# Kernel optimization log

Hardware: AMD Instinct MI355X
Metric: run time of the kernel (lower is better)

Reference implementation:

```python
import jax, jax.numpy as jnp
import numpy as np

N_SPK, M_UTT, D_EMB = 1024, 32, 512


def setup_inputs() -> dict:
    key = jax.random.key(0)
    k0, = jax.random.split(key, 1)
    embeddings = jax.random.normal(k0, (N_SPK, M_UTT, D_EMB), dtype=jnp.float32)
    return {
        "embeddings": embeddings,
        "w": jnp.asarray(5.0, dtype=jnp.float32),
        "b": jnp.asarray(1.0, dtype=jnp.float32),
        "N": N_SPK,
        "M": M_UTT,
    }


def reference(embeddings, w, b, N, M):
    # embeddings: [N, M, D]
    centroids = embeddings.mean(axis=1)          # [N, D]
    sum_ = embeddings.sum(axis=1)                # [N, D]
    e_flat = embeddings.reshape(N * M, -1)       # [NM, D]
    cosine_sim = e_flat @ centroids.T            # [NM, N]

    # Exclusive-centroid diagonal overwrite (faithful to source, including
    # the operator precedence: c_j = sum_[j] - e[j,k] / (1 - M)):
    #   diag[j,k] = (sum_[j] - e[j,k]/(1-M)) . e[j,k]
    inv = 1.0 / (1.0 - M)
    diag = (jnp.einsum('nmd,nd->nm', embeddings, sum_)
            - inv * jnp.sum(embeddings * embeddings, axis=-1))  # [N, M]

    rows = jnp.arange(N * M)
    cols = jnp.repeat(jnp.arange(N), M)          # label layout: [0]*M, [1]*M, ...
    cosine_sim = cosine_sim.at[rows, cols].set(diag.reshape(-1))

    logits = w * cosine_sim + b                  # [NM, N]
    # cross_entropy with labels = cols, mean reduction
    logz = jax.nn.logsumexp(logits, axis=-1)     # [NM]
    loss = jnp.mean(logz - logits[rows, cols])
    return loss
```

## Files before the change

kernel.cpp:

```cpp
#include <hip/hip_runtime.h>

#define N_SPK 1024
#define M_UTT 32
#define D_EMB 512
#define NROWS (N_SPK * M_UTT)

#define NEG_INF (-__builtin_inff())
#define MARGIN 25.0f

using f32x4 = __attribute__((ext_vector_type(4))) float;


__global__ __launch_bounds__(256)
void prep_kernel(const float* __restrict__ e,
                 float* __restrict__ sumf, float* __restrict__ ssqA,
                 float* __restrict__ dgl, float* __restrict__ c2A,
                 const float* __restrict__ wp, const float* __restrict__ bp,
                 float* __restrict__ out, int* __restrict__ count,
                 int* __restrict__ doneCnt) {
    __shared__ float csum[4][D_EMB];
    __shared__ float c2red[4];
    const int n = blockIdx.x;
    const int wv = threadIdx.x >> 6, l = threadIdx.x & 63;

    if (n == 0 && threadIdx.x == 0) { out[0] = 0.f; *count = 0; *doneCnt = 0; }

    float xs[8][8];
    float ssq[8];
    float cacc[8];
#pragma unroll
    for (int j = 0; j < 8; ++j) cacc[j] = 0.f;

#pragma unroll
    for (int mi = 0; mi < 8; ++mi) {
        const int m = mi * 4 + wv;
        const size_t row = (size_t)n * M_UTT + m;
        const float* p = e + row * D_EMB + l * 8;
        float4 x0 = *(const float4*)p;
        float4 x1 = *(const float4*)(p + 4);
        xs[mi][0] = x0.x; xs[mi][1] = x0.y; xs[mi][2] = x0.z; xs[mi][3] = x0.w;
        xs[mi][4] = x1.x; xs[mi][5] = x1.y; xs[mi][6] = x1.z; xs[mi][7] = x1.w;
        float sq = 0.f;
#pragma unroll
        for (int j = 0; j < 8; ++j) {
            float x = xs[mi][j];
            cacc[j] += x;
            sq = __builtin_fmaf(x, x, sq);
        }
#pragma unroll
        for (int off = 32; off; off >>= 1) sq += __shfl_xor(sq, off);
        ssq[mi] = sq;
        if (l == 0) ssqA[row] = sq;
    }

#pragma unroll
    for (int j = 0; j < 8; ++j) csum[wv][l * 8 + j] = cacc[j];
    __syncthreads();
    float c2acc = 0.f;
    for (int d = threadIdx.x; d < D_EMB; d += 256) {
        float s = csum[0][d] + csum[1][d] + csum[2][d] + csum[3][d];
        csum[0][d] = s;
        sumf[(size_t)n * D_EMB + d] = s;
        float c = s * (1.0f / M_UTT);
        c2acc = __builtin_fmaf(c, c, c2acc);
    }
#pragma unroll
    for (int off = 32; off; off >>= 1) c2acc += __shfl_xor(c2acc, off);
    if (l == 0) c2red[wv] = c2acc;
    __syncthreads();
    if (threadIdx.x == 0)
        c2A[n] = (c2red[0] + c2red[1]) + (c2red[2] + c2red[3]);

    float sv[8];
#pragma unroll
    for (int j = 0; j < 8; ++j) sv[j] = csum[0][l * 8 + j];
    const float w = wp[0], bb = bp[0];
#pragma unroll
    for (int mi = 0; mi < 8; ++mi) {
        float dg = 0.f;
#pragma unroll
        for (int j = 0; j < 8; ++j) dg = __builtin_fmaf(xs[mi][j], sv[j], dg);
#pragma unroll
        for (int off = 32; off; off >>= 1) dg += __shfl_xor(dg, off);
        if (l == 0) {
            const size_t row = (size_t)n * M_UTT + mi * 4 + wv;
            dgl[row] = __builtin_fmaf(w, dg + ssq[mi] * (1.0f / 31.0f), bb);
        }
    }
}

__global__ __launch_bounds__(256)
void select_kernel(const float* __restrict__ ssqA, const float* __restrict__ dgl,
                   const float* __restrict__ c2A,
                   const float* __restrict__ wp, const float* __restrict__ bp,
                   int* __restrict__ count, int* __restrict__ active) {
    __shared__ float red[4];
    float m = 0.f;
#pragma unroll
    for (int i = 0; i < 4; ++i)
        m = fmaxf(m, c2A[threadIdx.x + i * 256]);
#pragma unroll
    for (int off = 32; off; off >>= 1) m = fmaxf(m, __shfl_xor(m, off));
    if ((threadIdx.x & 63) == 0) red[threadIdx.x >> 6] = m;
    __syncthreads();
    const float c2 = fmaxf(fmaxf(red[0], red[1]), fmaxf(red[2], red[3]));
    const float Cmax = __builtin_sqrtf(c2);

    const int row = blockIdx.x * 256 + threadIdx.x;
    const float bound = __builtin_fmaf(
        __builtin_fabsf(wp[0]) * __builtin_sqrtf(ssqA[row]), Cmax, bp[0]);
    if (dgl[row] - bound < MARGIN) {
        int slot = atomicAdd(count, 1);
        active[slot] = row;
    }
}

__global__ __launch_bounds__(256)
void active_kernel(const float* __restrict__ e, const float* __restrict__ sumf,
                   const float* __restrict__ dgl,
                   const int* __restrict__ count, const int* __restrict__ active,
                   const float* __restrict__ wp, const float* __restrict__ bp,
                   float2* __restrict__ pmA, int* __restrict__ doneCnt,
                   float* __restrict__ out) {
    __shared__ float er[D_EMB];
    __shared__ float2 red2[4];
    __shared__ int lastFlag;
    const int tid = threadIdx.x;
    const int cnt = *count;
    if (cnt == 0) return;
    const float w = wp[0], bb = bp[0];

    const int xcd = blockIdx.x & 7;
    const int chunk = xcd >> 1;
    const int g = (blockIdx.x >> 3) * 2 + (xcd & 1);
    const int gstride = (gridDim.x >> 3) * 2;

    if (tid == 0) lastFlag = 0;
    int myItems = 0;

    for (int slot = g; slot < cnt; slot += gstride) {
        const int row = active[slot];
        __syncthreads();
        er[tid] = e[(size_t)row * D_EMB + tid];
        er[tid + 256] = e[(size_t)row * D_EMB + 256 + tid];
        __syncthreads();

        const int j = chunk * 256 + tid;
        const float* sp = sumf + (size_t)j * D_EMB;
        float d0 = 0.f, d1 = 0.f, d2 = 0.f, d3 = 0.f;
        for (int k = 0; k < D_EMB; k += 4) {
            float4 s4 = *(const float4*)(sp + k);
            d0 = __builtin_fmaf(er[k + 0], s4.x, d0);
            d1 = __builtin_fmaf(er[k + 1], s4.y, d1);
            d2 = __builtin_fmaf(er[k + 2], s4.z, d2);
            d3 = __builtin_fmaf(er[k + 3], s4.w, d3);
        }
        const float dot = (d0 + d1) + (d2 + d3);
        float lg = __builtin_fmaf(w, dot * (1.0f / M_UTT), bb);
        if (j == (row >> 5)) lg = dgl[row];

        float mx = lg;
#pragma unroll
        for (int off = 32; off; off >>= 1) mx = fmaxf(mx, __shfl_xor(mx, off));
        float ss = __expf(lg - mx);
#pragma unroll
        for (int off = 32; off; off >>= 1) ss += __shfl_xor(ss, off);
        if ((tid & 63) == 0) { float2 v; v.x = mx; v.y = ss; red2[tid >> 6] = v; }
        __syncthreads();
        if (tid == 0) {
            float M = fmaxf(fmaxf(red2[0].x, red2[1].x),
                            fmaxf(red2[2].x, red2[3].x));
            float S = red2[0].y * __expf(red2[0].x - M)
                    + red2[1].y * __expf(red2[1].x - M)
                    + red2[2].y * __expf(red2[2].x - M)
                    + red2[3].y * __expf(red2[3].x - M);
            float2 v; v.x = M; v.y = S;
            __hip_atomic_store((unsigned long long*)&pmA[slot * 4 + chunk],
                               __builtin_bit_cast(unsigned long long, v),
                               __ATOMIC_RELAXED, __HIP_MEMORY_SCOPE_AGENT);
        }
        ++myItems;
    }

    __syncthreads();
    if (tid == 0 && myItems > 0) {
        int old = __hip_atomic_fetch_add(doneCnt, myItems,
                                         __ATOMIC_ACQ_REL,
                                         __HIP_MEMORY_SCOPE_AGENT);
        if (old + myItems == cnt * 4) lastFlag = 1;
    }
    __syncthreads();

    if (lastFlag) {
        for (int slot = tid; slot < cnt; slot += 256) {
            float2 pm[4];
#pragma unroll
            for (int c = 0; c < 4; ++c) {
                unsigned long long bits = __hip_atomic_load(
                    (unsigned long long*)&pmA[slot * 4 + c],
                    __ATOMIC_RELAXED, __HIP_MEMORY_SCOPE_AGENT);
                pm[c] = __builtin_bit_cast(float2, bits);
            }
            float M = fmaxf(fmaxf(pm[0].x, pm[1].x), fmaxf(pm[2].x, pm[3].x));
            float S = pm[0].y * __expf(pm[0].x - M) + pm[1].y * __expf(pm[1].x - M)
                    + pm[2].y * __expf(pm[2].x - M) + pm[3].y * __expf(pm[3].x - M);
            float loss = M + __logf(S) - dgl[active[slot]];
            atomicAdd(out, loss * (1.0f / NROWS));
        }
    }
}


__global__ void centroid_kernel(const float* __restrict__ e,
                                float* __restrict__ cent) {
    int gid = blockIdx.x * 256 + threadIdx.x;
    int n = gid >> 9;
    int d = gid & 511;
    const float* p = e + ((size_t)n * M_UTT) * D_EMB + d;
    float s = 0.f;
#pragma unroll
    for (int m = 0; m < M_UTT; ++m) s += p[(size_t)m * D_EMB];
    cent[gid] = s * (1.0f / M_UTT);
}

__global__ void normsq_kernel(const float* __restrict__ e,
                              float* __restrict__ nsq) {
    int wv = threadIdx.x >> 6;
    int lane = threadIdx.x & 63;
    int row = blockIdx.x * 4 + wv;
    const float* p = e + (size_t)row * D_EMB + lane;
    float s = 0.f;
#pragma unroll
    for (int j = 0; j < 8; ++j) { float x = p[j * 64]; s += x * x; }
#pragma unroll
    for (int off = 32; off; off >>= 1) s += __shfl_xor(s, off);
    if (lane == 0) nsq[row] = s;
}

#define BR 64
#define BC 128
#define BK 16
#define TR 4
#define TC 8

__global__ __launch_bounds__(256, 2)
void ge2e_main(const float* __restrict__ e, const float* __restrict__ cent,
               const float* __restrict__ nsq, const float* __restrict__ wp,
               const float* __restrict__ bp, float* __restrict__ partials) {
    __shared__ float As[BK][BR];
    __shared__ float Bs[BK][BC];
    __shared__ float diagLs[BR];
    __shared__ float red[16];

    const int tid = threadIdx.x;
    const int tx = tid & 15;
    const int ty = tid >> 4;
    const int blk = blockIdx.x;
    const int r0 = blk * BR;

    const float w = *wp;
    const float bb = *bp;

    float m_run[TR], s_run[TR];
#pragma unroll
    for (int i = 0; i < TR; ++i) { m_run[i] = NEG_INF; s_run[i] = 0.f; }

    const int a_row = tid >> 2;
    const int a_k   = (tid & 3) * 4;
    const int b_col = tid >> 1;
    const int b_k   = (tid & 1) * 8;

    for (int ct = 0; ct < N_SPK / BC; ++ct) {
        const int c0 = ct * BC;
        float acc[TR][TC];
#pragma unroll
        for (int i = 0; i < TR; ++i)
#pragma unroll
            for (int j = 0; j < TC; ++j) acc[i][j] = 0.f;

        for (int kk = 0; kk < D_EMB; kk += BK) {
            __syncthreads();
            {
                float4 av = *(const float4*)(e + (size_t)(r0 + a_row) * D_EMB + kk + a_k);
                As[a_k + 0][a_row] = av.x;
                As[a_k + 1][a_row] = av.y;
                As[a_k + 2][a_row] = av.z;
                As[a_k + 3][a_row] = av.w;
            }
            {
                const float* bp0 = cent + (size_t)(c0 + b_col) * D_EMB + kk + b_k;
                float4 bv0 = *(const float4*)(bp0);
                float4 bv1 = *(const float4*)(bp0 + 4);
                Bs[b_k + 0][b_col] = bv0.x;
                Bs[b_k + 1][b_col] = bv0.y;
                Bs[b_k + 2][b_col] = bv0.z;
                Bs[b_k + 3][b_col] = bv0.w;
                Bs[b_k + 4][b_col] = bv1.x;
                Bs[b_k + 5][b_col] = bv1.y;
                Bs[b_k + 6][b_col] = bv1.z;
                Bs[b_k + 7][b_col] = bv1.w;
            }
            __syncthreads();

#pragma unroll
            for (int k = 0; k < BK; ++k) {
                float4 a4 = *(const float4*)&As[k][ty * TR];
                float4 b4a = *(const float4*)&Bs[k][tx * TC];
                float4 b4b = *(const float4*)&Bs[k][tx * TC + 4];
                float av[TR] = {a4.x, a4.y, a4.z, a4.w};
                float bv[TC] = {b4a.x, b4a.y, b4a.z, b4a.w,
                                b4b.x, b4b.y, b4b.z, b4b.w};
#pragma unroll
                for (int i = 0; i < TR; ++i)
#pragma unroll
                    for (int j = 0; j < TC; ++j)
                        acc[i][j] = __builtin_fmaf(av[i], bv[j], acc[i][j]);
            }
        }

#pragma unroll
        for (int i = 0; i < TR; ++i) {
            const int grow = r0 + ty * TR + i;
            const int dcol = grow >> 5;
            float lv[TC];
#pragma unroll
            for (int j = 0; j < TC; ++j) {
                const int gcol = c0 + tx * TC + j;
                float v = acc[i][j];
                float lg;
                if (gcol == dcol) {
                    lg = __builtin_fmaf(w, __builtin_fmaf(32.0f, v,
                             (1.0f / 31.0f) * nsq[grow]), bb);
                    diagLs[ty * TR + i] = lg;
                } else {
                    lg = __builtin_fmaf(w, v, bb);
                }
                lv[j] = lg;
            }
            float mx = lv[0];
#pragma unroll
            for (int j = 1; j < TC; ++j) mx = fmaxf(mx, lv[j]);
#pragma unroll
            for (int off = 8; off; off >>= 1) mx = fmaxf(mx, __shfl_xor(mx, off));
            float ss = 0.f;
#pragma unroll
            for (int j = 0; j < TC; ++j) ss += __expf(lv[j] - mx);
#pragma unroll
            for (int off = 8; off; off >>= 1) ss += __shfl_xor(ss, off);
            float nm = fmaxf(m_run[i], mx);
            s_run[i] = s_run[i] * __expf(m_run[i] - nm) + ss * __expf(mx - nm);
            m_run[i] = nm;
        }
    }

    __syncthreads();
    if (tx == 0) {
        float part = 0.f;
#pragma unroll
        for (int i = 0; i < TR; ++i) {
            const int lr = ty * TR + i;
            part += m_run[i] + __logf(s_run[i]) - diagLs[lr];
        }
        red[ty] = part;
    }
    __syncthreads();
    if (tid == 0) {
        float t = 0.f;
#pragma unroll
        for (int i = 0; i < 16; ++i) t += red[i];
        partials[blk] = t;
    }
}

__global__ void reduce_kernel(const float* __restrict__ partials,
                              float* __restrict__ out) {
    __shared__ float red[4];
    int tid = threadIdx.x;
    float v = partials[tid] + partials[tid + 256];
#pragma unroll
    for (int off = 32; off; off >>= 1) v += __shfl_xor(v, off);
    if ((tid & 63) == 0) red[tid >> 6] = v;
    __syncthreads();
    if (tid == 0)
        out[0] = (red[0] + red[1] + red[2] + red[3]) * (1.0f / NROWS);
}


extern "C" void kernel_launch(void* const* d_in, const int* in_sizes, int n_in,
                              void* d_out, int out_size, void* d_ws, size_t ws_size,
                              hipStream_t stream) {
    const float* e  = (const float*)d_in[0];
    const float* wp = (const float*)d_in[1];
    const float* bp = (const float*)d_in[2];
    float* out = (float*)d_out;

    const size_t NEED_FAST = 3543048ull;

    if (ws_size >= NEED_FAST) {
        char* base = (char*)d_ws;
        float*  sumf    = (float*) (base);
        float*  ssqA    = (float*) (base + 2097152ull);
        float*  dgl     = (float*) (base + 2228224ull);
        int*    active  = (int*)   (base + 2359296ull);
        float2* pmA     = (float2*)(base + 2490368ull);
        float*  c2A     = (float*) (base + 3538944ull);
        int*    count   = (int*)   (base + 3543040ull);
        int*    doneCnt = (int*)   (base + 3543044ull);

        prep_kernel<<<N_SPK, 256, 0, stream>>>(e, sumf, ssqA, dgl, c2A,
                                               wp, bp, out, count, doneCnt);
        select_kernel<<<NROWS / 256, 256, 0, stream>>>(ssqA, dgl, c2A,
                                                       wp, bp, count, active);
        active_kernel<<<512, 256, 0, stream>>>(e, sumf, dgl, count, active,
                                               wp, bp, pmA, doneCnt, out);
    } else {
        float* ws = (float*)d_ws;
        float* cent     = ws;
        float* nsq      = ws + 524288;
        float* partials = ws + 524288 + 32768;

        centroid_kernel<<<N_SPK * D_EMB / 256, 256, 0, stream>>>(e, cent);
        normsq_kernel<<<NROWS / 4, 256, 0, stream>>>(e, nsq);
        ge2e_main<<<NROWS / BR, 256, 0, stream>>>(e, cent, nsq, wp, bp, partials);
        reduce_kernel<<<1, 256, 0, stream>>>(partials, out);
    }
}
```

Before: 123.5 us.

## Split active-row logsumexp across 16 single-wave blocks per row

Restructures active_kernel from 256-thread blocks covering 4 column chunks into 64-thread single-wavefront blocks, each covering one of 16 chunks of 64 speaker columns. This removes the intra-block shared-memory reduction and its barrier, and spreads the work over more, smaller blocks. The cost is a larger partial (max, sum) buffer with 16 entries per active row, a bigger workspace requirement, and a final merge that reads four times as many partials. Each block also reloads the embedding row into shared memory for every slot, so the same row is now loaded 16 times instead of 4.

New measurement: 118.0 us. 1.05x faster.

```diff
diff --git a/kernel.cpp b/kernel.cpp
--- a/kernel.cpp
+++ b/kernel.cpp
@@ -115,37 +115,36 @@
     }
 }
 
-__global__ __launch_bounds__(256)
+__global__ __launch_bounds__(64)
 void active_kernel(const float* __restrict__ e, const float* __restrict__ sumf,
                    const float* __restrict__ dgl,
                    const int* __restrict__ count, const int* __restrict__ active,
                    const float* __restrict__ wp, const float* __restrict__ bp,
-                   float2* __restrict__ pmA, int* __restrict__ doneCnt,
+                   float2* __restrict__ pm16, int* __restrict__ doneCnt,
                    float* __restrict__ out) {
     __shared__ float er[D_EMB];
-    __shared__ float2 red2[4];
     __shared__ int lastFlag;
     const int tid = threadIdx.x;
     const int cnt = *count;
     if (cnt == 0) return;
     const float w = wp[0], bb = bp[0];
 
-    const int xcd = blockIdx.x & 7;
-    const int chunk = xcd >> 1;
-    const int g = (blockIdx.x >> 3) * 2 + (xcd & 1);
-    const int gstride = (gridDim.x >> 3) * 2;
+    const int g16 = blockIdx.x & 15;
+    const int slot0 = blockIdx.x >> 4;
+    const int gstride = gridDim.x >> 4;
 
     if (tid == 0) lastFlag = 0;
     int myItems = 0;
 
-    for (int slot = g; slot < cnt; slot += gstride) {
+    for (int slot = slot0; slot < cnt; slot += gstride) {
         const int row = active[slot];
         __syncthreads();
-        er[tid] = e[(size_t)row * D_EMB + tid];
-        er[tid + 256] = e[(size_t)row * D_EMB + 256 + tid];
+#pragma unroll
+        for (int i = 0; i < 8; ++i)
+            er[tid + i * 64] = e[(size_t)row * D_EMB + tid + i * 64];
         __syncthreads();
 
-        const int j = chunk * 256 + tid;
+        const int j = g16 * 64 + tid;
         const float* sp = sumf + (size_t)j * D_EMB;
         float d0 = 0.f, d1 = 0.f, d2 = 0.f, d3 = 0.f;
         for (int k = 0; k < D_EMB; k += 4) {
@@ -165,17 +164,9 @@
         float ss = __expf(lg - mx);
 #pragma unroll
         for (int off = 32; off; off >>= 1) ss += __shfl_xor(ss, off);
-        if ((tid & 63) == 0) { float2 v; v.x = mx; v.y = ss; red2[tid >> 6] = v; }
-        __syncthreads();
         if (tid == 0) {
-            float M = fmaxf(fmaxf(red2[0].x, red2[1].x),
-                            fmaxf(red2[2].x, red2[3].x));
-            float S = red2[0].y * __expf(red2[0].x - M)
-                    + red2[1].y * __expf(red2[1].x - M)
-                    + red2[2].y * __expf(red2[2].x - M)
-                    + red2[3].y * __expf(red2[3].x - M);
-            float2 v; v.x = M; v.y = S;
-            __hip_atomic_store((unsigned long long*)&pmA[slot * 4 + chunk],
+            float2 v; v.x = mx; v.y = ss;
+            __hip_atomic_store((unsigned long long*)&pm16[slot * 16 + g16],
                                __builtin_bit_cast(unsigned long long, v),
                                __ATOMIC_RELAXED, __HIP_MEMORY_SCOPE_AGENT);
         }
@@ -187,19 +178,38 @@
         int old = __hip_atomic_fetch_add(doneCnt, myItems,
                                          __ATOMIC_ACQ_REL,
                                          __HIP_MEMORY_SCOPE_AGENT);
-        if (old + myItems == cnt * 4) lastFlag = 1;
+        if (old + myItems == cnt * 16) lastFlag = 1;
     }
     __syncthreads();
 
     if (lastFlag) {
-        for (int slot = tid; slot < cnt; slot += 256) {
+        for (int slot = tid; slot < cnt; slot += 64) {
             float2 pm[4];
 #pragma unroll
             for (int c = 0; c < 4; ++c) {
-                unsigned long long bits = __hip_atomic_load(
-                    (unsigned long long*)&pmA[slot * 4 + c],
+                float2 r0, r1, r2, r3;
+                unsigned long long b0 = __hip_atomic_load(
+                    (unsigned long long*)&pm16[slot * 16 + 4 * c + 0],
                     __ATOMIC_RELAXED, __HIP_MEMORY_SCOPE_AGENT);
-                pm[c] = __builtin_bit_cast(float2, bits);
+                unsigned long long b1 = __hip_atomic_load(
+                    (unsigned long long*)&pm16[slot * 16 + 4 * c + 1],
+                    __ATOMIC_RELAXED, __HIP_MEMORY_SCOPE_AGENT);
+                unsigned long long b2 = __hip_atomic_load(
+                    (unsigned long long*)&pm16[slot * 16 + 4 * c + 2],
+                    __ATOMIC_RELAXED, __HIP_MEMORY_SCOPE_AGENT);
+                unsigned long long b3 = __hip_atomic_load(
+                    (unsigned long long*)&pm16[slot * 16 + 4 * c + 3],
+                    __ATOMIC_RELAXED, __HIP_MEMORY_SCOPE_AGENT);
+                r0 = __builtin_bit_cast(float2, b0);
+                r1 = __builtin_bit_cast(float2, b1);
+                r2 = __builtin_bit_cast(float2, b2);
+                r3 = __builtin_bit_cast(float2, b3);
+                float M = fmaxf(fmaxf(r0.x, r1.x), fmaxf(r2.x, r3.x));
+                float S = r0.y * __expf(r0.x - M)
+                        + r1.y * __expf(r1.x - M)
+                        + r2.y * __expf(r2.x - M)
+                        + r3.y * __expf(r3.x - M);
+                pm[c].x = M; pm[c].y = S;
             }
             float M = fmaxf(fmaxf(pm[0].x, pm[1].x), fmaxf(pm[2].x, pm[3].x));
             float S = pm[0].y * __expf(pm[0].x - M) + pm[1].y * __expf(pm[1].x - M)
@@ -394,7 +404,7 @@
     const float* bp = (const float*)d_in[2];
     float* out = (float*)d_out;
 
-    const size_t NEED_FAST = 3543048ull;
+    const size_t NEED_FAST = 6688776ull;
 
     if (ws_size >= NEED_FAST) {
         char* base = (char*)d_ws;
@@ -402,17 +412,17 @@
         float*  ssqA    = (float*) (base + 2097152ull);
         float*  dgl     = (float*) (base + 2228224ull);
         int*    active  = (int*)   (base + 2359296ull);
-        float2* pmA     = (float2*)(base + 2490368ull);
-        float*  c2A     = (float*) (base + 3538944ull);
-        int*    count   = (int*)   (base + 3543040ull);
-        int*    doneCnt = (int*)   (base + 3543044ull);
+        float2* pm16    = (float2*)(base + 2490368ull);
+        float*  c2A     = (float*) (base + 6684672ull);
+        int*    count   = (int*)   (base + 6688768ull);
+        int*    doneCnt = (int*)   (base + 6688772ull);
 
         prep_kernel<<<N_SPK, 256, 0, stream>>>(e, sumf, ssqA, dgl, c2A,
                                                wp, bp, out, count, doneCnt);
         select_kernel<<<NROWS / 256, 256, 0, stream>>>(ssqA, dgl, c2A,
                                                        wp, bp, count, active);
-        active_kernel<<<512, 256, 0, stream>>>(e, sumf, dgl, count, active,
-                                               wp, bp, pmA, doneCnt, out);
+        active_kernel<<<1024, 64, 0, stream>>>(e, sumf, dgl, count, active,
+                                               wp, bp, pm16, doneCnt, out);
     } else {
         float* ws = (float*)d_ws;
         float* cent     = ws;
```
